# Kernel tuning notes

Hardware: AMD Instinct MI355X
Metric: run time of the kernel (lower is better)

Reference implementation:

```python
import jax, jax.numpy as jnp
import numpy as np


def setup_inputs() -> dict:
    key = jax.random.key(0)
    kq, kk, kv = jax.random.split(key, 3)
    B, S, H, D = 2, 2048, 16, 64
    q = jax.random.normal(kq, (B, S, H, D), dtype=jnp.float32)
    k = jax.random.normal(kk, (B, S, H, D), dtype=jnp.float32)
    v = jax.random.normal(kv, (B, S, H, D), dtype=jnp.float32)
    # additive key padding mask, [B,1,1,K]; 0 = unmasked, -inf = masked
    key_padding_mask = jnp.zeros((B, 1, 1, S), dtype=jnp.float32)
    return {"q": q, "k": k, "v": v, "key_padding_mask": key_padding_mask}


def reference(q, k, v, key_padding_mask):
    # q,k,v: [B, S, H, D]; key_padding_mask: [B,1,1,K] additive
    head_dim = q.shape[-1]
    softmax_scale = 1.0 / np.sqrt(head_dim).astype(np.float32)
    # [B, H, Q, K] logits with additive mask
    logits = jnp.einsum('bqhd,bkhd->bhqk', q, k) * softmax_scale + key_padding_mask
    attn = jax.nn.softmax(logits, axis=-1)
    # dropout p=0.0 -> identity in eval mode
    out = jnp.einsum('bhqk,bkhd->bqhd', attn, v)
    return out
```

## Files before the change

### kernel.cpp

```cpp
#include <hip/hip_runtime.h>


typedef __attribute__((ext_vector_type(8))) short bf16x8;
typedef __attribute__((ext_vector_type(4))) short bf16x4;
typedef __attribute__((ext_vector_type(4))) float f32x4;

#define B_ 2
#define S_ 2048
#define H_ 16
#define D_ 64
#define BQ 128
#define BK 64
#define LDK 72
#define ROWSZ (H_ * D_)

__device__ __forceinline__ ushort f2bs(float f) {
    union { float f; unsigned u; } x; x.f = f;
    unsigned r = (x.u + 0x7FFFu + ((x.u >> 16) & 1u)) >> 16;
    return (ushort)r;
}

__device__ __forceinline__ unsigned pack2(float a, float b) {
#if __has_builtin(__builtin_amdgcn_cvt_pk_bf16_f32)
    typedef __attribute__((ext_vector_type(2))) __bf16 hwbf2;
    union { hwbf2 v; unsigned u; } x;
    x.v = __builtin_amdgcn_cvt_pk_bf16_f32(a, b);
    return x.u;
#else
    return (unsigned)f2bs(a) | ((unsigned)f2bs(b) << 16);
#endif
}

__device__ __forceinline__ float fexp2(float x) {
#if __has_builtin(__builtin_amdgcn_exp2f)
    return __builtin_amdgcn_exp2f(x);
#else
    return __expf(x * 0.69314718055994531f);
#endif
}

__device__ __forceinline__ f32x4 mfma16(bf16x4 a, bf16x4 b, f32x4 c) {
#if __has_builtin(__builtin_amdgcn_mfma_f32_16x16x16bf16_1k)
    return __builtin_amdgcn_mfma_f32_16x16x16bf16_1k(a, b, c, 0, 0, 0);
#else
    bf16x8 a8 = {a[0], a[1], a[2], a[3], 0, 0, 0, 0};
    bf16x8 b8 = {b[0], b[1], b[2], b[3], 0, 0, 0, 0};
    return __builtin_amdgcn_mfma_f32_16x16x32_bf16(a8, b8, c, 0, 0, 0);
#endif
}

__global__ __launch_bounds__(512, 4)
void fattn_kernel(const float* __restrict__ qg,
                  const float* __restrict__ kg,
                  const float* __restrict__ vg,
                  const float* __restrict__ maskg,
                  float* __restrict__ outg)
{
    __shared__ ushort Ks[BK * LDK];
    __shared__ ushort Vt[D_ * LDK];

    const int qt = blockIdx.x;
    const int h  = blockIdx.y;
    const int b  = blockIdx.z;

    const int tid = threadIdx.x;
    const int w   = tid >> 6;
    const int lane = tid & 63;
    const int g   = lane >> 4;
    const int l15 = lane & 15;

    const size_t kvbase = (size_t)b * S_ * ROWSZ + h * D_;

    const int qrow = qt * BQ + w * 16 + l15;
    const float* qp = qg + (size_t)(b * S_ + qrow) * ROWSZ + h * D_;
    bf16x8 qf[2];
#pragma unroll
    for (int half = 0; half < 2; ++half) {
        float4 f0 = *(const float4*)(qp + half * 32 + g * 8);
        float4 f1 = *(const float4*)(qp + half * 32 + g * 8 + 4);
        union { bf16x8 v; uint4 u; } x;
        x.u = make_uint4(pack2(f0.x, f0.y), pack2(f0.z, f0.w),
                         pack2(f1.x, f1.y), pack2(f1.z, f1.w));
        qf[half] = x.v;
    }

    const int skey16 = tid >> 4;
    const int sd4    = (tid & 15) * 4;
    const int svd    = tid & 63;
    const int svk8   = (tid >> 6) * 8;

    float m_r = -1e30f, l_r = 0.0f;
    f32x4 o_acc[4];
#pragma unroll
    for (int t = 0; t < 4; ++t) o_acc[t] = (f32x4){0.f, 0.f, 0.f, 0.f};

    const float SCALE2 = 0.125f * 1.44269504088896340736f;
    const float LOG2E  = 1.44269504088896340736f;
    const float* maskb = maskg + (size_t)b * S_;

    for (int kt = 0; kt < S_ / BK; ++kt) {
#pragma unroll
        for (int pass = 0; pass < 2; ++pass) {
            int key = skey16 + pass * 32;
            float4 f = *(const float4*)(kg + kvbase + (size_t)(kt * BK + key) * ROWSZ + sd4);
            *(uint2*)&Ks[key * LDK + sd4] = make_uint2(pack2(f.x, f.y), pack2(f.z, f.w));
        }
        {
            float vv[8];
#pragma unroll
            for (int i = 0; i < 8; ++i)
                vv[i] = vg[kvbase + (size_t)(kt * BK + svk8 + i) * ROWSZ + svd];
            union { bf16x8 v; uint4 u; } x;
            x.u = make_uint4(pack2(vv[0], vv[1]), pack2(vv[2], vv[3]),
                             pack2(vv[4], vv[5]), pack2(vv[6], vv[7]));
            *(bf16x8*)&Vt[svd * LDK + svk8] = x.v;
        }
        __syncthreads();

        f32x4 sacc[4];
#pragma unroll
        for (int t = 0; t < 4; ++t) {
            f32x4 acc = (f32x4){0.f, 0.f, 0.f, 0.f};
            bf16x8 kf0 = *(const bf16x8*)&Ks[(t * 16 + l15) * LDK + 0  + g * 8];
            bf16x8 kf1 = *(const bf16x8*)&Ks[(t * 16 + l15) * LDK + 32 + g * 8];
            acc = __builtin_amdgcn_mfma_f32_16x16x32_bf16(kf0, qf[0], acc, 0, 0, 0);
            acc = __builtin_amdgcn_mfma_f32_16x16x32_bf16(kf1, qf[1], acc, 0, 0, 0);
            sacc[t] = acc;
        }

        float sv[4][4];
#pragma unroll
        for (int t = 0; t < 4; ++t) {
            float4 mk = *(const float4*)(maskb + kt * BK + t * 16 + g * 4);
            sv[t][0] = fmaf(mk.x, LOG2E, sacc[t][0] * SCALE2);
            sv[t][1] = fmaf(mk.y, LOG2E, sacc[t][1] * SCALE2);
            sv[t][2] = fmaf(mk.z, LOG2E, sacc[t][2] * SCALE2);
            sv[t][3] = fmaf(mk.w, LOG2E, sacc[t][3] * SCALE2);
        }

        float cm = sv[0][0];
#pragma unroll
        for (int t = 0; t < 4; ++t)
#pragma unroll
            for (int r = 0; r < 4; ++r) cm = fmaxf(cm, sv[t][r]);
        cm = fmaxf(cm, __shfl_xor(cm, 16));
        cm = fmaxf(cm, __shfl_xor(cm, 32));
        float newm = fmaxf(m_r, cm);
        float alpha = fexp2(m_r - newm);
        float rs = 0.f;
#pragma unroll
        for (int t = 0; t < 4; ++t)
#pragma unroll
            for (int r = 0; r < 4; ++r) {
                float p = fexp2(sv[t][r] - newm);
                sv[t][r] = p;
                rs += p;
            }
        rs += __shfl_xor(rs, 16);
        rs += __shfl_xor(rs, 32);
        l_r = l_r * alpha + rs;
        m_r = newm;
#pragma unroll
        for (int t = 0; t < 4; ++t) {
            o_acc[t][0] *= alpha; o_acc[t][1] *= alpha;
            o_acc[t][2] *= alpha; o_acc[t][3] *= alpha;
        }

        bf16x4 pf[4];
#pragma unroll
        for (int c = 0; c < 4; ++c) {
            union { bf16x4 v; uint2 u; } x;
            x.u = make_uint2(pack2(sv[c][0], sv[c][1]), pack2(sv[c][2], sv[c][3]));
            pf[c] = x.v;
        }

#pragma unroll
        for (int t2 = 0; t2 < 4; ++t2)
#pragma unroll
            for (int c = 0; c < 4; ++c) {
                bf16x4 vf = *(const bf16x4*)&Vt[(t2 * 16 + l15) * LDK + c * 16 + g * 4];
                o_acc[t2] = mfma16(vf, pf[c], o_acc[t2]);
            }
        __syncthreads();
    }

    const float inv = 1.0f / l_r;
    float* op = outg + (size_t)(b * S_ + qrow) * ROWSZ + h * D_;
#pragma unroll
    for (int t2 = 0; t2 < 4; ++t2)
#pragma unroll
        for (int r = 0; r < 4; ++r)
            op[t2 * 16 + g * 4 + r] = o_acc[t2][r] * inv;
}

extern "C" void kernel_launch(void* const* d_in, const int* in_sizes, int n_in,
                              void* d_out, int out_size, void* d_ws, size_t ws_size,
                              hipStream_t stream) {
    dim3 grid(S_ / BQ, H_, B_);
    fattn_kernel<<<grid, dim3(512), 0, stream>>>(
        (const float*)d_in[0], (const float*)d_in[1], (const float*)d_in[2],
        (const float*)d_in[3], (float*)d_out);
}
```

Baseline: 175.6 us.

## Double-buffer K/V tiles with register prefetch and fold scale/mask into MFMA

Adds double-buffered shared K/V tiles. The next tile's global loads are issued into registers before the current tile's compute and written to the other buffer afterwards, so one barrier per iteration suffices and load latency overlaps MFMA work. The softmax scale is folded into Q at load time, and the log2e-scaled mask is preloaded into shared memory and used as the MFMA accumulator's initial value. The row-sum shuffles are deferred to the end, and V is stored in a permuted layout so it can be read with wider 16-byte LDS loads. In exchange it uses more shared memory and registers, which could reduce occupancy.

```diff
diff --git a/kernel.cpp b/kernel.cpp
--- a/kernel.cpp
+++ b/kernel.cpp
@@ -1,4 +1,5 @@
 #include <hip/hip_runtime.h>
+#include <hip/hip_bf16.h>
 
 
 typedef __attribute__((ext_vector_type(8))) short bf16x8;
@@ -11,24 +12,17 @@
 #define D_ 64
 #define BQ 128
 #define BK 64
+#define NT (S_ / BK)
 #define LDK 72
 #define ROWSZ (H_ * D_)
 
-__device__ __forceinline__ ushort f2bs(float f) {
-    union { float f; unsigned u; } x; x.f = f;
-    unsigned r = (x.u + 0x7FFFu + ((x.u >> 16) & 1u)) >> 16;
-    return (ushort)r;
-}
+#define LOG2E  1.44269504088896340736f
+#define SCALE2 (0.125f * LOG2E)
 
 __device__ __forceinline__ unsigned pack2(float a, float b) {
-#if __has_builtin(__builtin_amdgcn_cvt_pk_bf16_f32)
-    typedef __attribute__((ext_vector_type(2))) __bf16 hwbf2;
-    union { hwbf2 v; unsigned u; } x;
-    x.v = __builtin_amdgcn_cvt_pk_bf16_f32(a, b);
+    union { __hip_bfloat162 h; unsigned u; } x;
+    x.h = __float22bfloat162_rn(make_float2(a, b));
     return x.u;
-#else
-    return (unsigned)f2bs(a) | ((unsigned)f2bs(b) << 16);
-#endif
 }
 
 __device__ __forceinline__ float fexp2(float x) {
@@ -56,20 +50,19 @@
                   const float* __restrict__ maskg,
                   float* __restrict__ outg)
 {
-    __shared__ ushort Ks[BK * LDK];
-    __shared__ ushort Vt[D_ * LDK];
-
-    const int qt = blockIdx.x;
-    const int h  = blockIdx.y;
-    const int b  = blockIdx.z;
-
+    __shared__ __attribute__((aligned(16))) ushort Ks[2][BK * LDK];
+    __shared__ __attribute__((aligned(16))) ushort Vt[2][D_ * LDK];
+    __shared__ __attribute__((aligned(16))) float  Em[S_];
+
+    const int qt = blockIdx.x, h = blockIdx.y, b = blockIdx.z;
     const int tid = threadIdx.x;
-    const int w   = tid >> 6;
-    const int lane = tid & 63;
-    const int g   = lane >> 4;
-    const int l15 = lane & 15;
-
-    const size_t kvbase = (size_t)b * S_ * ROWSZ + h * D_;
+    const int w = tid >> 6, lane = tid & 63, g = lane >> 4, l15 = lane & 15;
+
+    {
+        float4 mv = *(const float4*)(maskg + (size_t)b * S_ + tid * 4);
+        *(float4*)&Em[tid * 4] = make_float4(mv.x * LOG2E, mv.y * LOG2E,
+                                             mv.z * LOG2E, mv.w * LOG2E);
+    }
 
     const int qrow = qt * BQ + w * 16 + l15;
     const float* qp = qg + (size_t)(b * S_ + qrow) * ROWSZ + h * D_;
@@ -79,63 +72,66 @@
         float4 f0 = *(const float4*)(qp + half * 32 + g * 8);
         float4 f1 = *(const float4*)(qp + half * 32 + g * 8 + 4);
         union { bf16x8 v; uint4 u; } x;
-        x.u = make_uint4(pack2(f0.x, f0.y), pack2(f0.z, f0.w),
-                         pack2(f1.x, f1.y), pack2(f1.z, f1.w));
+        x.u = make_uint4(pack2(f0.x * SCALE2, f0.y * SCALE2),
+                         pack2(f0.z * SCALE2, f0.w * SCALE2),
+                         pack2(f1.x * SCALE2, f1.y * SCALE2),
+                         pack2(f1.z * SCALE2, f1.w * SCALE2));
         qf[half] = x.v;
     }
 
     const int skey16 = tid >> 4;
     const int sd4    = (tid & 15) * 4;
-    const int svd    = tid & 63;
-    const int svk8   = (tid >> 6) * 8;
+    const int svd    = lane;
+    const int svk8   = w * 8;
+    const int vc0 = (w >> 1) * 4 + 16 * ((2 * w) & 3);
+    const int vc1 = (w >> 1) * 4 + 16 * ((2 * w + 1) & 3);
+
+    const size_t kvbase = (size_t)b * S_ * ROWSZ + h * D_;
+
+    float4 kpre0, kpre1;
+    float  vpre[8];
+    auto prefetch = [&](int kt) {
+        const float* kb = kg + kvbase + (size_t)kt * BK * ROWSZ;
+        kpre0 = *(const float4*)(kb + (size_t)skey16 * ROWSZ + sd4);
+        kpre1 = *(const float4*)(kb + (size_t)(skey16 + 32) * ROWSZ + sd4);
+        const float* vb = vg + kvbase + (size_t)kt * BK * ROWSZ + svd;
+#pragma unroll
+        for (int i = 0; i < 8; ++i) vpre[i] = vb[(size_t)(svk8 + i) * ROWSZ];
+    };
+    auto stage = [&](int buf) {
+        *(uint2*)&Ks[buf][skey16 * LDK + sd4] =
+            make_uint2(pack2(kpre0.x, kpre0.y), pack2(kpre0.z, kpre0.w));
+        *(uint2*)&Ks[buf][(skey16 + 32) * LDK + sd4] =
+            make_uint2(pack2(kpre1.x, kpre1.y), pack2(kpre1.z, kpre1.w));
+        *(uint2*)&Vt[buf][svd * LDK + vc0] =
+            make_uint2(pack2(vpre[0], vpre[1]), pack2(vpre[2], vpre[3]));
+        *(uint2*)&Vt[buf][svd * LDK + vc1] =
+            make_uint2(pack2(vpre[4], vpre[5]), pack2(vpre[6], vpre[7]));
+    };
 
     float m_r = -1e30f, l_r = 0.0f;
     f32x4 o_acc[4];
 #pragma unroll
     for (int t = 0; t < 4; ++t) o_acc[t] = (f32x4){0.f, 0.f, 0.f, 0.f};
 
-    const float SCALE2 = 0.125f * 1.44269504088896340736f;
-    const float LOG2E  = 1.44269504088896340736f;
-    const float* maskb = maskg + (size_t)b * S_;
-
-    for (int kt = 0; kt < S_ / BK; ++kt) {
-#pragma unroll
-        for (int pass = 0; pass < 2; ++pass) {
-            int key = skey16 + pass * 32;
-            float4 f = *(const float4*)(kg + kvbase + (size_t)(kt * BK + key) * ROWSZ + sd4);
-            *(uint2*)&Ks[key * LDK + sd4] = make_uint2(pack2(f.x, f.y), pack2(f.z, f.w));
-        }
-        {
-            float vv[8];
-#pragma unroll
-            for (int i = 0; i < 8; ++i)
-                vv[i] = vg[kvbase + (size_t)(kt * BK + svk8 + i) * ROWSZ + svd];
-            union { bf16x8 v; uint4 u; } x;
-            x.u = make_uint4(pack2(vv[0], vv[1]), pack2(vv[2], vv[3]),
-                             pack2(vv[4], vv[5]), pack2(vv[6], vv[7]));
-            *(bf16x8*)&Vt[svd * LDK + svk8] = x.v;
-        }
-        __syncthreads();
-
-        f32x4 sacc[4];
+    prefetch(0);
+    stage(0);
+    __syncthreads();
+
+    for (int kt = 0; kt < NT; ++kt) {
+        const int cur = kt & 1;
+        if (kt + 1 < NT) prefetch(kt + 1);
+
+        const ushort* ks = Ks[cur];
+        float sv[4][4];
 #pragma unroll
         for (int t = 0; t < 4; ++t) {
-            f32x4 acc = (f32x4){0.f, 0.f, 0.f, 0.f};
-            bf16x8 kf0 = *(const bf16x8*)&Ks[(t * 16 + l15) * LDK + 0  + g * 8];
-            bf16x8 kf1 = *(const bf16x8*)&Ks[(t * 16 + l15) * LDK + 32 + g * 8];
+            f32x4 acc = *(const f32x4*)&Em[kt * BK + t * 16 + g * 4];
+            bf16x8 kf0 = *(const bf16x8*)&ks[(t * 16 + l15) * LDK + g * 8];
+            bf16x8 kf1 = *(const bf16x8*)&ks[(t * 16 + l15) * LDK + 32 + g * 8];
             acc = __builtin_amdgcn_mfma_f32_16x16x32_bf16(kf0, qf[0], acc, 0, 0, 0);
             acc = __builtin_amdgcn_mfma_f32_16x16x32_bf16(kf1, qf[1], acc, 0, 0, 0);
-            sacc[t] = acc;
-        }
-
-        float sv[4][4];
-#pragma unroll
-        for (int t = 0; t < 4; ++t) {
-            float4 mk = *(const float4*)(maskb + kt * BK + t * 16 + g * 4);
-            sv[t][0] = fmaf(mk.x, LOG2E, sacc[t][0] * SCALE2);
-            sv[t][1] = fmaf(mk.y, LOG2E, sacc[t][1] * SCALE2);
-            sv[t][2] = fmaf(mk.z, LOG2E, sacc[t][2] * SCALE2);
-            sv[t][3] = fmaf(mk.w, LOG2E, sacc[t][3] * SCALE2);
+            sv[t][0] = acc[0]; sv[t][1] = acc[1]; sv[t][2] = acc[2]; sv[t][3] = acc[3];
         }
 
         float cm = sv[0][0];
@@ -145,8 +141,8 @@
             for (int r = 0; r < 4; ++r) cm = fmaxf(cm, sv[t][r]);
         cm = fmaxf(cm, __shfl_xor(cm, 16));
         cm = fmaxf(cm, __shfl_xor(cm, 32));
-        float newm = fmaxf(m_r, cm);
-        float alpha = fexp2(m_r - newm);
+        const float newm = fmaxf(m_r, cm);
+        const float alpha = fexp2(m_r - newm);
         float rs = 0.f;
 #pragma unroll
         for (int t = 0; t < 4; ++t)
@@ -156,8 +152,6 @@
                 sv[t][r] = p;
                 rs += p;
             }
-        rs += __shfl_xor(rs, 16);
-        rs += __shfl_xor(rs, 32);
         l_r = l_r * alpha + rs;
         m_r = newm;
 #pragma unroll
@@ -174,16 +168,25 @@
             pf[c] = x.v;
         }
 
-#pragma unroll
-        for (int t2 = 0; t2 < 4; ++t2)
-#pragma unroll
-            for (int c = 0; c < 4; ++c) {
-                bf16x4 vf = *(const bf16x4*)&Vt[(t2 * 16 + l15) * LDK + c * 16 + g * 4];
-                o_acc[t2] = mfma16(vf, pf[c], o_acc[t2]);
+        const ushort* vt = Vt[cur];
+#pragma unroll
+        for (int t2 = 0; t2 < 4; ++t2) {
+#pragma unroll
+            for (int c2 = 0; c2 < 2; ++c2) {
+                bf16x8 vv = *(const bf16x8*)&vt[(t2 * 16 + l15) * LDK + g * 16 + c2 * 8];
+                bf16x4 vlo = {vv[0], vv[1], vv[2], vv[3]};
+                bf16x4 vhi = {vv[4], vv[5], vv[6], vv[7]};
+                o_acc[t2] = mfma16(vlo, pf[2 * c2],     o_acc[t2]);
+                o_acc[t2] = mfma16(vhi, pf[2 * c2 + 1], o_acc[t2]);
             }
+        }
+
+        if (kt + 1 < NT) stage(cur ^ 1);
         __syncthreads();
     }
 
+    l_r += __shfl_xor(l_r, 16);
+    l_r += __shfl_xor(l_r, 32);
     const float inv = 1.0f / l_r;
     float* op = outg + (size_t)(b * S_ + qrow) * ROWSZ + h * D_;
 #pragma unroll
```

New measurement: 155.1 us. -11.7%, faster.
